# Performance work log

Measured on AMD Instinct MI355X. Metric: run time of the kernel, lower is better.

The kernel has to match this reference:

```python
import jax, jax.numpy as jnp
import numpy as np

B, S, D = 64, 8192, 32  # batch, sequence length, feature size (in_size == out_size == 32)


def setup_inputs() -> dict:
    key = jax.random.key(0)
    kx, kq, kk, kv = jax.random.split(key, 4)
    x = jax.random.normal(kx, (B, S, D), dtype=jnp.float32)
    Wq = jax.random.normal(kq, (1, D, D), dtype=jnp.float32)
    Wk = jax.random.normal(kk, (1, D, D), dtype=jnp.float32)
    Wv = jax.random.normal(kv, (1, D, D), dtype=jnp.float32)
    return {"x": x, "Wq": Wq, "Wk": Wk, "Wv": Wv}


def reference(x, Wq, Wk, Wv):
    # Projections: [B,S,D] @ [1,D,D] -> [B,S,D] (broadcast over batch)
    q = jnp.matmul(x, Wq)
    k = jnp.matmul(x, Wk)
    v = jnp.matmul(x, Wv)
    # Transposed attention: scores = softmax(Q^T K, dim=1) over feature dims -> [B,D,D]
    scores = jax.nn.softmax(jnp.einsum('bsq,bsk->bqk', q, k), axis=1)
    # out = scores @ V^T -> [B,D,S]
    out = jnp.einsum('bqk,bsk->bqs', scores, v)
    return out
```

## Files before the change

### kernel.cpp

```cpp
#include <hip/hip_runtime.h>
#include <math.h>

#define B_ 64
#define S_ 8192
#define D_ 32

__device__ __forceinline__ void load_lds16(const float* g, float* l) {
    __builtin_amdgcn_global_load_lds(
        (const __attribute__((address_space(1))) void*)g,
        (__attribute__((address_space(3))) void*)l,
        16, 0, 0);
}

#define GR_SUB 256

__global__ __launch_bounds__(256) void gram_k(const float* __restrict__ x,
                                              float* __restrict__ gpart) {
    __shared__ float tile[GR_SUB * D_];
    const int blk = blockIdx.x;
    const int b   = blk >> 3;
    const int ch8 = blk & 7;
    const int t   = threadIdx.x;
    const int w   = t >> 6;
    const int l   = t & 63;
    const int i0  = ((l >> 3) & 7) << 2;
    const int j0  = (l & 7) << 2;

    const float* xb = x + ((size_t)b * S_ + (size_t)ch8 * 1024) * D_;

    float acc[4][4] = {};
    for (int sub = 0; sub < 4; ++sub) {
        const float* src = xb + (size_t)sub * GR_SUB * D_;
        #pragma unroll
        for (int k = 0; k < 8; ++k) {
            const int g = k * 256 + t;
            load_lds16(src + g * 4, tile + g * 4);
        }
        __syncthreads();

        const int rbase = w * 64;
        #pragma unroll 4
        for (int rr = 0; rr < 64; ++rr) {
            const int r = rbase + rr;
            const float4 xi = *(const float4*)(tile + r * D_ + i0);
            const float4 xj = *(const float4*)(tile + r * D_ + j0);
            const float xiv[4] = {xi.x, xi.y, xi.z, xi.w};
            const float xjv[4] = {xj.x, xj.y, xj.z, xj.w};
            #pragma unroll
            for (int a = 0; a < 4; ++a)
                #pragma unroll
                for (int c = 0; c < 4; ++c)
                    acc[a][c] = fmaf(xiv[a], xjv[c], acc[a][c]);
        }
        __syncthreads();
    }

    float* red = tile;
    #pragma unroll
    for (int a = 0; a < 4; ++a)
        #pragma unroll
        for (int c = 0; c < 4; ++c)
            red[w * 1024 + l * 16 + a * 4 + c] = acc[a][c];
    __syncthreads();

    #pragma unroll
    for (int e = t; e < 1024; e += 256) {
        const float s = red[e] + red[1024 + e] + red[2048 + e] + red[3072 + e];
        const int ll = e >> 4, ee = e & 15;
        const int i = (((ll >> 3) & 7) << 2) + (ee >> 2);
        const int j = ((ll & 7) << 2) + (ee & 3);
        gpart[(size_t)blk * 1024 + i * 32 + j] = s;
    }
}

#define K1_CH 8
__global__ __launch_bounds__(1024) void attn_small(const float* __restrict__ gpart,
                                                   const float* __restrict__ Wq,
                                                   const float* __restrict__ Wk,
                                                   const float* __restrict__ Wv,
                                                   float* __restrict__ M) {
    __shared__ float GL[32][33], WqL[32][33], WkL[32][33], WvL[32][33];
    __shared__ float T1L[32][33], PL[32][33];
    __shared__ float mcol[32], scol[32];

    const int b = blockIdx.x;
    const int t = threadIdx.x;
    const int r = t >> 5, c = t & 31;

    float g = 0.f;
    #pragma unroll
    for (int cc = 0; cc < K1_CH; ++cc)
        g += gpart[(size_t)(b * K1_CH + cc) * 1024 + t];
    GL[r][c]  = g;
    WqL[r][c] = Wq[t];
    WkL[r][c] = Wk[t];
    WvL[r][c] = Wv[t];
    __syncthreads();

    float t1 = 0.f;
    #pragma unroll
    for (int e = 0; e < 32; ++e) t1 = fmaf(GL[r][e], WkL[e][c], t1);
    T1L[r][c] = t1;
    __syncthreads();

    float p = 0.f;
    #pragma unroll
    for (int d = 0; d < 32; ++d) p = fmaf(WqL[d][r], T1L[d][c], p);
    PL[r][c] = p;
    __syncthreads();

    if (t < 32) {
        float m = -INFINITY;
        #pragma unroll
        for (int q = 0; q < 32; ++q) m = fmaxf(m, PL[q][t]);
        float s = 0.f;
        #pragma unroll
        for (int q = 0; q < 32; ++q) s += __expf(PL[q][t] - m);
        mcol[t] = m;
        scol[t] = 1.0f / s;
    }
    __syncthreads();
    const float sc = __expf(PL[r][c] - mcol[c]) * scol[c];
    PL[r][c] = sc;
    __syncthreads();

    float mm = 0.f;
    #pragma unroll
    for (int k = 0; k < 32; ++k) mm = fmaf(WvL[r][k], PL[c][k], mm);
    M[(size_t)b * 1024 + t] = mm;
}

#define OUT_ROWS 256

__global__ __launch_bounds__(256) void out_k(const float* __restrict__ x,
                                             const float* __restrict__ M,
                                             float* __restrict__ out) {
    __shared__ float tile[OUT_ROWS * D_];
    const int blk = blockIdx.x;
    const int b   = blk >> 5;
    const int ch  = blk & 31;
    const int t   = threadIdx.x;

    const float* src = x + ((size_t)b * S_ + (size_t)ch * OUT_ROWS) * D_;
    #pragma unroll
    for (int k = 0; k < 8; ++k) {
        const int g  = k * 256 + t;
        const int r  = g >> 3, j = g & 7;
        const int gs = r * 8 + (j ^ (r & 7));
        load_lds16(src + gs * 4, tile + g * 4);
    }
    __syncthreads();

    const float* Mb = M + (size_t)b * 1024;
    float acc[32] = {};
    const int r = t;
    #pragma unroll
    for (int j = 0; j < 8; ++j) {
        const int pg = r * 8 + (j ^ (r & 7));
        const float4 xv = *(const float4*)(tile + pg * 4);
        const float xd[4] = {xv.x, xv.y, xv.z, xv.w};
        #pragma unroll
        for (int dd = 0; dd < 4; ++dd) {
            const int d = j * 4 + dd;
            #pragma unroll
            for (int q = 0; q < 32; ++q)
                acc[q] = fmaf(Mb[d * 32 + q], xd[dd], acc[q]);
        }
    }

    const int s = ch * OUT_ROWS + r;
    float* ob = out + (size_t)b * D_ * S_ + s;
    #pragma unroll
    for (int q = 0; q < 32; ++q)
        ob[(size_t)q * S_] = acc[q];
}

extern "C" void kernel_launch(void* const* d_in, const int* in_sizes, int n_in,
                              void* d_out, int out_size, void* d_ws, size_t ws_size,
                              hipStream_t stream) {
    const float* x  = (const float*)d_in[0];
    const float* Wq = (const float*)d_in[1];
    const float* Wk = (const float*)d_in[2];
    const float* Wv = (const float*)d_in[3];
    float* out = (float*)d_out;

    float* gpart = (float*)d_ws;
    float* M     = gpart + (size_t)B_ * K1_CH * 1024;

    gram_k<<<B_ * K1_CH, 256, 0, stream>>>(x, gpart);
    attn_small<<<B_, 1024, 0, stream>>>(gpart, Wq, Wk, Wv, M);
    out_k<<<B_ * 32, 256, 0, stream>>>(x, M, out);
}
```

Before: 156.3 us.

## Restructure Gram kernel with 8x8 register tiles, double buffering, and swizzled LDS

The Gram-matrix kernel now gives each thread an 8x8 accumulator tile instead of 4x4, raising FLOPs per LDS load. Each block handles 512 rows and the grid doubles to 16 chunks per batch. Rows are staged through a double-buffered LDS tile with an XOR swizzle so the next sub-tile's async load overlaps compute and bank conflicts drop. Partial sums are first reduced across lane groups with shuffles before the LDS reduction. The risk is higher register pressure from 64 accumulators, plus more partials for attn_small to sum.

Result: slower. 159.7 us (+2.1%).

```diff
diff --git a/kernel.cpp b/kernel.cpp
--- a/kernel.cpp
+++ b/kernel.cpp
@@ -12,68 +12,107 @@
         16, 0, 0);
 }
 
-#define GR_SUB 256
+#define GCH 16
+#define GSUB 128
+#define GNSUB 4
 
 __global__ __launch_bounds__(256) void gram_k(const float* __restrict__ x,
                                               float* __restrict__ gpart) {
-    __shared__ float tile[GR_SUB * D_];
+    __shared__ float tile[2][GSUB * D_];
     const int blk = blockIdx.x;
-    const int b   = blk >> 3;
-    const int ch8 = blk & 7;
+    const int b   = blk >> 4;
+    const int ch  = blk & 15;
     const int t   = threadIdx.x;
     const int w   = t >> 6;
-    const int l   = t & 63;
-    const int i0  = ((l >> 3) & 7) << 2;
-    const int j0  = (l & 7) << 2;
-
-    const float* xb = x + ((size_t)b * S_ + (size_t)ch8 * 1024) * D_;
-
-    float acc[4][4] = {};
-    for (int sub = 0; sub < 4; ++sub) {
-        const float* src = xb + (size_t)sub * GR_SUB * D_;
-        #pragma unroll
-        for (int k = 0; k < 8; ++k) {
-            const int g = k * 256 + t;
-            load_lds16(src + g * 4, tile + g * 4);
+    const int lane = t & 63;
+    const int rg  = lane >> 4;
+    const int l16 = lane & 15;
+    const int bi  = (l16 >> 2) << 3;
+    const int bj  = (l16 & 3) << 3;
+    const int gi0 = bi >> 2;
+    const int gj0 = bj >> 2;
+
+    const float* xb = x + ((size_t)b * S_ + (size_t)ch * (GSUB * GNSUB)) * D_;
+
+    float acc[8][8] = {};
+
+    #pragma unroll
+    for (int it = 0; it < 4; ++it) {
+        const int p = it * 256 + t;
+        const int r = p >> 3, c = p & 7;
+        const int sg = r * 8 + (c ^ (r & 7));
+        load_lds16(xb + sg * 4, &tile[0][p * 4]);
+    }
+    __syncthreads();
+
+    for (int s = 0; s < GNSUB; ++s) {
+        if (s + 1 < GNSUB) {
+            const float* src = xb + (size_t)(s + 1) * GSUB * D_;
+            #pragma unroll
+            for (int it = 0; it < 4; ++it) {
+                const int p = it * 256 + t;
+                const int r = p >> 3, c = p & 7;
+                const int sg = r * 8 + (c ^ (r & 7));
+                load_lds16(src + sg * 4, &tile[(s + 1) & 1][p * 4]);
+            }
+        }
+        const float* tl = tile[s & 1];
+        #pragma unroll
+        for (int it = 0; it < 8; ++it) {
+            const int r  = w * 32 + it * 4 + rg;
+            const int sw = r & 7;
+            const float* row = tl + r * D_;
+            const float4 xiA = *(const float4*)(row + ((gi0 ^ sw) << 2));
+            const float4 xiB = *(const float4*)(row + (((gi0 + 1) ^ sw) << 2));
+            const float4 xjA = *(const float4*)(row + ((gj0 ^ sw) << 2));
+            const float4 xjB = *(const float4*)(row + (((gj0 + 1) ^ sw) << 2));
+            const float xi[8] = {xiA.x, xiA.y, xiA.z, xiA.w,
+                                 xiB.x, xiB.y, xiB.z, xiB.w};
+            const float xj[8] = {xjA.x, xjA.y, xjA.z, xjA.w,
+                                 xjB.x, xjB.y, xjB.z, xjB.w};
+            #pragma unroll
+            for (int a = 0; a < 8; ++a)
+                #pragma unroll
+                for (int c2 = 0; c2 < 8; ++c2)
+                    acc[a][c2] = fmaf(xi[a], xj[c2], acc[a][c2]);
         }
         __syncthreads();
-
-        const int rbase = w * 64;
-        #pragma unroll 4
-        for (int rr = 0; rr < 64; ++rr) {
-            const int r = rbase + rr;
-            const float4 xi = *(const float4*)(tile + r * D_ + i0);
-            const float4 xj = *(const float4*)(tile + r * D_ + j0);
-            const float xiv[4] = {xi.x, xi.y, xi.z, xi.w};
-            const float xjv[4] = {xj.x, xj.y, xj.z, xj.w};
-            #pragma unroll
-            for (int a = 0; a < 4; ++a)
-                #pragma unroll
-                for (int c = 0; c < 4; ++c)
-                    acc[a][c] = fmaf(xiv[a], xjv[c], acc[a][c]);
-        }
-        __syncthreads();
-    }
-
-    float* red = tile;
-    #pragma unroll
-    for (int a = 0; a < 4; ++a)
-        #pragma unroll
-        for (int c = 0; c < 4; ++c)
-            red[w * 1024 + l * 16 + a * 4 + c] = acc[a][c];
-    __syncthreads();
-
-    #pragma unroll
-    for (int e = t; e < 1024; e += 256) {
-        const float s = red[e] + red[1024 + e] + red[2048 + e] + red[3072 + e];
-        const int ll = e >> 4, ee = e & 15;
-        const int i = (((ll >> 3) & 7) << 2) + (ee >> 2);
-        const int j = ((ll & 7) << 2) + (ee & 3);
-        gpart[(size_t)blk * 1024 + i * 32 + j] = s;
-    }
-}
-
-#define K1_CH 8
+    }
+
+    #pragma unroll
+    for (int a = 0; a < 8; ++a)
+        #pragma unroll
+        for (int c2 = 0; c2 < 8; ++c2) {
+            float v = acc[a][c2];
+            v += __shfl_xor(v, 16, 64);
+            v += __shfl_xor(v, 32, 64);
+            acc[a][c2] = v;
+        }
+
+    float* red = &tile[0][0];
+    __syncthreads();
+    if (rg == 0) {
+        #pragma unroll
+        for (int a = 0; a < 8; ++a)
+            #pragma unroll
+            for (int c2 = 0; c2 < 8; c2 += 4) {
+                *(float4*)(red + w * 1024 + l16 * 64 + a * 8 + c2) =
+                    make_float4(acc[a][c2], acc[a][c2 + 1],
+                                acc[a][c2 + 2], acc[a][c2 + 3]);
+            }
+    }
+    __syncthreads();
+    #pragma unroll
+    for (int e4 = 0; e4 < 4; ++e4) {
+        const int e = e4 * 256 + t;
+        const float sv = red[e] + red[1024 + e] + red[2048 + e] + red[3072 + e];
+        const int li = e >> 6, a = (e >> 3) & 7, c2 = e & 7;
+        const int i = ((li >> 2) << 3) + a;
+        const int j = ((li & 3) << 3) + c2;
+        gpart[(size_t)blk * 1024 + i * 32 + j] = sv;
+    }
+}
+
 __global__ __launch_bounds__(1024) void attn_small(const float* __restrict__ gpart,
                                                    const float* __restrict__ Wq,
                                                    const float* __restrict__ Wk,
@@ -89,8 +128,8 @@
 
     float g = 0.f;
     #pragma unroll
-    for (int cc = 0; cc < K1_CH; ++cc)
-        g += gpart[(size_t)(b * K1_CH + cc) * 1024 + t];
+    for (int cc = 0; cc < GCH; ++cc)
+        g += gpart[(size_t)(b * GCH + cc) * 1024 + t];
     GL[r][c]  = g;
     WqL[r][c] = Wq[t];
     WkL[r][c] = Wk[t];
@@ -185,9 +224,9 @@
     float* out = (float*)d_out;
 
     float* gpart = (float*)d_ws;
-    float* M     = gpart + (size_t)B_ * K1_CH * 1024;
-
-    gram_k<<<B_ * K1_CH, 256, 0, stream>>>(x, gpart);
+    float* M     = gpart + (size_t)B_ * GCH * 1024;
+
+    gram_k<<<B_ * GCH, 256, 0, stream>>>(x, gpart);
     attn_small<<<B_, 1024, 0, stream>>>(gpart, Wq, Wk, Wv, M);
     out_k<<<B_ * 32, 256, 0, stream>>>(x, M, out);
 }
```
